# Kernel optimization log

Measured on AMD Instinct MI355X. Metric: run time of the kernel, lower is better.

## Reference

```python
import jax, jax.numpy as jnp
import numpy as np

B, S, H = 1, 2048, 1024          # batch, seq, hidden_size
INTER, K, DST, DTR = 2048, 4, 16, 64  # intermediate, kernel, ssm_state, dt_rank


def setup_inputs() -> dict:
    key = jax.random.key(0)
    ks = jax.random.split(key, 10)
    sc = 0.02
    return {
        "x": jax.random.normal(ks[0], (B, S, H), jnp.float32),
        "W_in": jax.random.normal(ks[1], (H, 2 * INTER), jnp.float32) * sc,
        "conv_w": jax.random.normal(ks[2], (K, 1, INTER), jnp.float32) * sc,
        "conv_b": jax.random.normal(ks[3], (INTER,), jnp.float32) * sc,
        "W_x": jax.random.normal(ks[4], (INTER, DTR + 2 * DST), jnp.float32) * sc,
        "W_dt": jax.random.normal(ks[5], (DTR, INTER), jnp.float32) * sc,
        "b_dt": jax.random.normal(ks[6], (INTER,), jnp.float32) * sc,
        "A_log": jax.random.normal(ks[7], (INTER, DST), jnp.float32) * sc,
        "D": jax.random.normal(ks[8], (INTER,), jnp.float32) * sc,
        "W_out": jax.random.normal(ks[9], (INTER, H), jnp.float32) * sc,
    }


def _ssm(dA, dBu, C):
    # dA, dBu: (b, s, h, d); C: (b, s, d) -> y: (b, s, h)
    xs = (jnp.moveaxis(dA, 1, 0), jnp.moveaxis(dBu, 1, 0), jnp.moveaxis(C, 1, 0))
    state0 = jnp.zeros(dA.shape[:1] + dA.shape[2:], dA.dtype)  # (b, h, d)

    def step(state, inp):
        Ai, dBui, Ci = inp  # (b,h,d), (b,h,d), (b,d)
        state = Ai * state + dBui
        y = jnp.einsum('bhd,bd->bh', state, Ci)
        return state, y

    _, ys = jax.lax.scan(step, state0, xs)  # ys: (s, b, h)
    return jnp.moveaxis(ys, 0, 1)


def reference(x, W_in, conv_w, conv_b, W_x, W_dt, b_dt, A_log, D, W_out):
    proj = x @ W_in                              # (b, s, 2*inter)
    raw, gate = jnp.split(proj, 2, axis=-1)      # each (b, s, inter)

    # causal depthwise conv over time, groups = inter
    conv = jax.lax.conv_general_dilated(
        raw, conv_w, window_strides=(1,), padding=[(K - 1, 0)],
        dimension_numbers=('NWC', 'WIO', 'NWC'), feature_group_count=INTER)
    h = jax.nn.silu(conv + conv_b)               # (b, s, inter)

    ssm_p = h @ W_x                              # (b, s, dtr + 2*d)
    ts, Bmat, C = jnp.split(ssm_p, [DTR, DTR + DST], axis=-1)
    dt = jax.nn.softplus(ts @ W_dt + b_dt)       # (b, s, inter)

    A = -jnp.exp(A_log)                          # (inter, d)
    dA = jnp.exp(dt[..., None] * A)              # (b, s, inter, d)
    dBu = dt[..., None] * Bmat[:, :, None, :] * h[..., None]  # (b, s, inter, d)

    y = _ssm(dA, dBu, C)                         # (b, s, inter)
    y = y + h * D
    y = y * jax.nn.silu(gate)
    return y @ W_out                             # (b, s, hidden)
```

## Files before the change

### kernel.cpp

```cpp
#include <hip/hip_runtime.h>
#include <math.h>

#define SEQ   2048
#define HID   1024
#define INTER 2048
#define DST   16
#define DTR   64
#define NP    96
#define NC    64
#define LCH   32
#define KS    16

typedef _Float16 f16;
typedef _Float16 f16x8 __attribute__((ext_vector_type(8)));
typedef _Float16 f16x4v __attribute__((ext_vector_type(4)));
typedef float f32x4 __attribute__((ext_vector_type(4)));

__device__ __forceinline__ float sigmoidf_(float x) { return 1.0f / (1.0f + expf(-x)); }
__device__ __forceinline__ float siluf_(float x)    { return x * sigmoidf_(x); }
__device__ __forceinline__ float softplusf_(float x){ return (x > 20.0f) ? x : log1pf(expf(x)); }

__global__ __launch_bounds__(256) void cvt_f16(const float* __restrict__ in,
                                               f16* __restrict__ out)
{
    int i = (blockIdx.x * 256 + threadIdx.x) * 4;
    float4 v = *(const float4*)&in[i];
    f16x4v o;
    o.x = (f16)v.x; o.y = (f16)v.y; o.z = (f16)v.z; o.w = (f16)v.w;
    *(f16x4v*)&out[i] = o;
}

__global__ __launch_bounds__(256) void transpose_f16(const float* __restrict__ W,
                                                     f16* __restrict__ Wt,
                                                     int K, int N)
{
    __shared__ float t[32][33];
    const int n0 = blockIdx.x * 32, k0 = blockIdx.y * 32;
    const int j = threadIdx.x & 31, i0 = threadIdx.x >> 5;
#pragma unroll
    for (int r = 0; r < 4; ++r)
        t[i0 + r * 8][j] = W[(size_t)(k0 + i0 + r * 8) * N + n0 + j];
    __syncthreads();
#pragma unroll
    for (int r = 0; r < 4; ++r)
        Wt[(size_t)(n0 + i0 + r * 8) * K + k0 + j] = (f16)t[j][i0 + r * 8];
}

template<int BM, int BN, int KK>
__global__ __launch_bounds__(256) void gemm_f16mfma(const f16* __restrict__ Ah,
                                                    const f16* __restrict__ Bt,
                                                    float* __restrict__ C,
                                                    int N)
{
    constexpr int BK = 64;
    __shared__ __align__(16) f16 As[BM * BK];
    __shared__ __align__(16) f16 Bs[BN * BK];

    const int tid = threadIdx.x;
    const int wid = tid >> 6, lane = tid & 63;
    const int wr = wid >> 1, wc = wid & 1;
    const int m0 = blockIdx.y * BM, n0 = blockIdx.x * BN;
    const int l15 = lane & 15, lhi = lane >> 4;

    constexpr int MR = BM / 32;
    constexpr int NR = BN / 32;

    f32x4 acc[MR][NR] = {};

    for (int k0 = 0; k0 < KK; k0 += BK) {
        constexpr int CA = BM * BK * 2 / 1024;
#pragma unroll
        for (int c0 = 0; c0 < CA; c0 += 4) {
            int c = c0 + wid;
            int e = c * 64 + lane;
            int row = e >> 3, seg = e & 7;
            __builtin_amdgcn_global_load_lds(
                (const __attribute__((address_space(1))) unsigned int*)
                    (Ah + (size_t)(m0 + row) * KK + k0 + seg * 8),
                (__attribute__((address_space(3))) unsigned int*)(As + c * 512),
                16, 0, 0);
        }
        constexpr int CB = BN * BK * 2 / 1024;
#pragma unroll
        for (int c0 = 0; c0 < CB; c0 += 4) {
            int c = c0 + wid;
            int e = c * 64 + lane;
            int row = e >> 3, seg = e & 7;
            __builtin_amdgcn_global_load_lds(
                (const __attribute__((address_space(1))) unsigned int*)
                    (Bt + (size_t)(n0 + row) * KK + k0 + seg * 8),
                (__attribute__((address_space(3))) unsigned int*)(Bs + c * 512),
                16, 0, 0);
        }
        __syncthreads();

#pragma unroll
        for (int kk = 0; kk < BK; kk += 32) {
            f16x8 af[MR], bf[NR];
#pragma unroll
            for (int i = 0; i < MR; ++i)
                af[i] = *(const f16x8*)&As[(wr * (BM / 2) + i * 16 + l15) * BK + kk + lhi * 8];
#pragma unroll
            for (int n = 0; n < NR; ++n)
                bf[n] = *(const f16x8*)&Bs[(wc * (BN / 2) + n * 16 + l15) * BK + kk + lhi * 8];
#pragma unroll
            for (int i = 0; i < MR; ++i)
#pragma unroll
                for (int n = 0; n < NR; ++n)
                    acc[i][n] = __builtin_amdgcn_mfma_f32_16x16x32_f16(af[i], bf[n], acc[i][n], 0, 0, 0);
        }
        __syncthreads();
    }

#pragma unroll
    for (int i = 0; i < MR; ++i)
#pragma unroll
        for (int n = 0; n < NR; ++n)
#pragma unroll
            for (int r = 0; r < 4; ++r)
                C[(size_t)(m0 + wr * (BM / 2) + i * 16 + lhi * 4 + r) * N
                  + n0 + wc * (BN / 2) + n * 16 + l15] = acc[i][n][r];
}

__global__ __launch_bounds__(256) void hwx_mfma(const f16* __restrict__ hh,
                                                const f16* __restrict__ WxT,
                                                float* __restrict__ partials)
{
    constexpr int BM = 128, BN = 96, BK = 64;
    __shared__ __align__(16) f16 As[BM * BK];
    __shared__ __align__(16) f16 Bs[BN * BK];

    const int tid = threadIdx.x;
    const int wid = tid >> 6, lane = tid & 63;
    const int wr = wid >> 1, wc = wid & 1;
    const int m0 = blockIdx.x * BM;
    const int ks = blockIdx.y;
    const int l15 = lane & 15, lhi = lane >> 4;

    constexpr int MR = 4, NR = 3;
    f32x4 acc[MR][NR] = {};

    for (int k0 = ks * 128; k0 < ks * 128 + 128; k0 += BK) {
#pragma unroll
        for (int c0 = 0; c0 < 16; c0 += 4) {
            int c = c0 + wid;
            int e = c * 64 + lane;
            int row = e >> 3, seg = e & 7;
            __builtin_amdgcn_global_load_lds(
                (const __attribute__((address_space(1))) unsigned int*)
                    (hh + (size_t)(m0 + row) * INTER + k0 + seg * 8),
                (__attribute__((address_space(3))) unsigned int*)(As + c * 512),
                16, 0, 0);
        }
#pragma unroll
        for (int c0 = 0; c0 < 12; c0 += 4) {
            int c = c0 + wid;
            int e = c * 64 + lane;
            int row = e >> 3, seg = e & 7;
            __builtin_amdgcn_global_load_lds(
                (const __attribute__((address_space(1))) unsigned int*)
                    (WxT + (size_t)row * INTER + k0 + seg * 8),
                (__attribute__((address_space(3))) unsigned int*)(Bs + c * 512),
                16, 0, 0);
        }
        __syncthreads();

#pragma unroll
        for (int kk = 0; kk < BK; kk += 32) {
            f16x8 af[MR], bf[NR];
#pragma unroll
            for (int i = 0; i < MR; ++i)
                af[i] = *(const f16x8*)&As[(wr * 64 + i * 16 + l15) * BK + kk + lhi * 8];
#pragma unroll
            for (int n = 0; n < NR; ++n)
                bf[n] = *(const f16x8*)&Bs[(wc * 48 + n * 16 + l15) * BK + kk + lhi * 8];
#pragma unroll
            for (int i = 0; i < MR; ++i)
#pragma unroll
                for (int n = 0; n < NR; ++n)
                    acc[i][n] = __builtin_amdgcn_mfma_f32_16x16x32_f16(af[i], bf[n], acc[i][n], 0, 0, 0);
        }
        __syncthreads();
    }

    float* P = partials + (size_t)ks * (SEQ * NP);
#pragma unroll
    for (int i = 0; i < MR; ++i)
#pragma unroll
        for (int n = 0; n < NR; ++n)
#pragma unroll
            for (int r = 0; r < 4; ++r)
                P[(size_t)(m0 + wr * 64 + i * 16 + lhi * 4 + r) * NP
                  + wc * 48 + n * 16 + l15] = acc[i][n][r];
}

__global__ __launch_bounds__(256) void reduce_partials(const float* __restrict__ partials,
                                                       float* __restrict__ ssm_p,
                                                       f16* __restrict__ tsh)
{
    int i = blockIdx.x * 256 + threadIdx.x;
    if (i < SEQ * NP) {
        float a = 0.0f;
#pragma unroll
        for (int c = 0; c < KS; ++c) a += partials[(size_t)c * (SEQ * NP) + i];
        ssm_p[i] = a;
        int j = i % NP;
        if (j < DTR) tsh[(size_t)(i / NP) * DTR + j] = (f16)a;
    }
}

__global__ __launch_bounds__(256) void dt_mfma(const f16* __restrict__ tsh,
                                               const f16* __restrict__ WdtT,
                                               const float* __restrict__ bdt,
                                               float* __restrict__ dtb)
{
    constexpr int BM = 128, BN = 128, BK = 64;
    __shared__ __align__(16) f16 As[BM * BK];
    __shared__ __align__(16) f16 Bs[BN * BK];

    const int tid = threadIdx.x;
    const int wid = tid >> 6, lane = tid & 63;
    const int wr = wid >> 1, wc = wid & 1;
    const int m0 = blockIdx.y * BM, n0 = blockIdx.x * BN;
    const int l15 = lane & 15, lhi = lane >> 4;

    constexpr int MR = 4, NR = 4;
    f32x4 acc[MR][NR] = {};

#pragma unroll
    for (int c0 = 0; c0 < 16; c0 += 4) {
        int c = c0 + wid;
        int e = c * 64 + lane;
        int row = e >> 3, seg = e & 7;
        __builtin_amdgcn_global_load_lds(
            (const __attribute__((address_space(1))) unsigned int*)
                (tsh + (size_t)(m0 + row) * DTR + seg * 8),
            (__attribute__((address_space(3))) unsigned int*)(As + c * 512),
            16, 0, 0);
        __builtin_amdgcn_global_load_lds(
            (const __attribute__((address_space(1))) unsigned int*)
                (WdtT + (size_t)(n0 + row) * DTR + seg * 8),
            (__attribute__((address_space(3))) unsigned int*)(Bs + c * 512),
            16, 0, 0);
    }
    __syncthreads();

#pragma unroll
    for (int kk = 0; kk < 64; kk += 32) {
        f16x8 af[MR], bf[NR];
#pragma unroll
        for (int i = 0; i < MR; ++i)
            af[i] = *(const f16x8*)&As[(wr * 64 + i * 16 + l15) * BK + kk + lhi * 8];
#pragma unroll
        for (int n = 0; n < NR; ++n)
            bf[n] = *(const f16x8*)&Bs[(wc * 64 + n * 16 + l15) * BK + kk + lhi * 8];
#pragma unroll
        for (int i = 0; i < MR; ++i)
#pragma unroll
            for (int n = 0; n < NR; ++n)
                acc[i][n] = __builtin_amdgcn_mfma_f32_16x16x32_f16(af[i], bf[n], acc[i][n], 0, 0, 0);
    }

#pragma unroll
    for (int i = 0; i < MR; ++i)
#pragma unroll
        for (int n = 0; n < NR; ++n) {
            int col = n0 + wc * 64 + n * 16 + l15;
            float bv = bdt[col];
#pragma unroll
            for (int r = 0; r < 4; ++r)
                dtb[(size_t)(m0 + wr * 64 + i * 16 + lhi * 4 + r) * INTER + col] =
                    softplusf_(acc[i][n][r] + bv);
        }
}

__global__ __launch_bounds__(256) void conv_silu(const float* __restrict__ proj,
                                                 const float* __restrict__ cw,
                                                 const float* __restrict__ cb,
                                                 float* __restrict__ hbuf,
                                                 f16* __restrict__ hh)
{
    int idx = blockIdx.x * 256 + threadIdx.x;
    int c4 = (idx & (INTER / 4 - 1)) * 4;
    int s = idx >> 9;
    float4 acc = *(const float4*)&cb[c4];
#pragma unroll
    for (int k = 0; k < 4; ++k) {
        int sp = s + k - 3;
        if (sp >= 0) {
            float4 p = *(const float4*)&proj[(size_t)sp * (2 * INTER) + c4];
            float4 w = *(const float4*)&cw[k * INTER + c4];
            acc.x = fmaf(p.x, w.x, acc.x);
            acc.y = fmaf(p.y, w.y, acc.y);
            acc.z = fmaf(p.z, w.z, acc.z);
            acc.w = fmaf(p.w, w.w, acc.w);
        }
    }
    float4 o;
    o.x = siluf_(acc.x); o.y = siluf_(acc.y); o.z = siluf_(acc.z); o.w = siluf_(acc.w);
    *(float4*)&hbuf[(size_t)idx * 4] = o;
    f16x4v h4;
    h4.x = (f16)o.x; h4.y = (f16)o.y; h4.z = (f16)o.z; h4.w = (f16)o.w;
    *(f16x4v*)&hh[(size_t)idx * 4] = h4;
}

__global__ __launch_bounds__(256) void ssm_pass1(const float* __restrict__ dtb,
                                                 const float* __restrict__ hbuf,
                                                 const float* __restrict__ ssm_p,
                                                 const float* __restrict__ A_log,
                                                 float* __restrict__ Sbuf,
                                                 float* __restrict__ Pbuf)
{
    const int h = blockIdx.x * 256 + threadIdx.x;
    const int c = blockIdx.y;
    const int s0 = c * LCH;

    __shared__ float Bs[LCH][DST];
    for (int j = threadIdx.x; j < LCH * DST; j += 256) {
        int r = j >> 4, dd = j & 15;
        Bs[r][dd] = ssm_p[(size_t)(s0 + r) * NP + DTR + dd];
    }
    __syncthreads();

    float A[DST], st[DST], P[DST];
#pragma unroll
    for (int d = 0; d < DST; ++d) {
        A[d] = -__expf(A_log[(size_t)h * DST + d]);
        st[d] = 0.0f;
        P[d] = 1.0f;
    }

    for (int r = 0; r < LCH; ++r) {
        float dtv = dtb[(size_t)(s0 + r) * INTER + h];
        float hv  = hbuf[(size_t)(s0 + r) * INTER + h];
        float dh = dtv * hv;
#pragma unroll
        for (int d = 0; d < DST; ++d) {
            float da = __expf(dtv * A[d]);
            st[d] = fmaf(da, st[d], dh * Bs[r][d]);
            P[d] *= da;
        }
    }

    size_t base = ((size_t)c * INTER + h) * DST;
#pragma unroll
    for (int d = 0; d < DST; d += 4) {
        *(float4*)&Sbuf[base + d] = make_float4(st[d], st[d+1], st[d+2], st[d+3]);
        *(float4*)&Pbuf[base + d] = make_float4(P[d], P[d+1], P[d+2], P[d+3]);
    }
}

__global__ __launch_bounds__(256) void ssm_pass2(const float* __restrict__ Sbuf,
                                                 const float* __restrict__ Pbuf,
                                                 float* __restrict__ Cin)
{
    int i = blockIdx.x * 256 + threadIdx.x;
    float carry = 0.0f;
    for (int c = 0; c < NC; ++c) {
        size_t idx = (size_t)c * (INTER * DST) + i;
        Cin[idx] = carry;
        carry = fmaf(Pbuf[idx], carry, Sbuf[idx]);
    }
}

__global__ __launch_bounds__(256) void ssm_pass3(const float* __restrict__ dtb,
                                                 const float* __restrict__ hbuf,
                                                 const float* __restrict__ ssm_p,
                                                 const float* __restrict__ proj,
                                                 const float* __restrict__ A_log,
                                                 const float* __restrict__ Dvec,
                                                 const float* __restrict__ Cin,
                                                 f16* __restrict__ yh)
{
    const int h = blockIdx.x * 256 + threadIdx.x;
    const int c = blockIdx.y;
    const int s0 = c * LCH;

    __shared__ float Bs[LCH][DST];
    __shared__ float Cs[LCH][DST];
    for (int j = threadIdx.x; j < LCH * DST; j += 256) {
        int r = j >> 4, dd = j & 15;
        Bs[r][dd] = ssm_p[(size_t)(s0 + r) * NP + DTR + dd];
        Cs[r][dd] = ssm_p[(size_t)(s0 + r) * NP + DTR + DST + dd];
    }
    __syncthreads();

    float A[DST], st[DST];
    size_t base = ((size_t)c * INTER + h) * DST;
#pragma unroll
    for (int d = 0; d < DST; ++d) {
        A[d] = -__expf(A_log[(size_t)h * DST + d]);
        st[d] = Cin[base + d];
    }
    const float Dv = Dvec[h];

    for (int r = 0; r < LCH; ++r) {
        float dtv = dtb[(size_t)(s0 + r) * INTER + h];
        float hv  = hbuf[(size_t)(s0 + r) * INTER + h];
        float g   = proj[(size_t)(s0 + r) * (2 * INTER) + INTER + h];
        float dh = dtv * hv;
        float y = 0.0f;
#pragma unroll
        for (int d = 0; d < DST; ++d) {
            float da = __expf(dtv * A[d]);
            st[d] = fmaf(da, st[d], dh * Bs[r][d]);
            y = fmaf(st[d], Cs[r][d], y);
        }
        y = fmaf(hv, Dv, y);
        yh[(size_t)(s0 + r) * INTER + h] = (f16)(y * siluf_(g));
    }
}

extern "C" void kernel_launch(void* const* d_in, const int* in_sizes, int n_in,
                              void* d_out, int out_size, void* d_ws, size_t ws_size,
                              hipStream_t stream)
{
    const float* x      = (const float*)d_in[0];
    const float* W_in   = (const float*)d_in[1];
    const float* conv_w = (const float*)d_in[2];
    const float* conv_b = (const float*)d_in[3];
    const float* W_x    = (const float*)d_in[4];
    const float* W_dt   = (const float*)d_in[5];
    const float* b_dt   = (const float*)d_in[6];
    const float* A_log  = (const float*)d_in[7];
    const float* Dv     = (const float*)d_in[8];
    const float* W_out  = (const float*)d_in[9];
    float* out = (float*)d_out;

    float* ws = (float*)d_ws;
    float* proj  = ws;
    float* hbuf  = ws + 8388608;
    float* dtb   = ws + 12582912;
    float* ssm_p = ws + 16777216;
    float* parts = ws + 16973824;
    float* Sbuf  = ws + 20119552;
    float* Pbuf  = ws + 22216704;
    float* Cin   = ws + 24313856;
    f16* yh      = (f16*)(ws + 16973824);
    f16* W_out_t = (f16*)(ws + 19070976);
    f16* xh      = (f16*)(ws + 20119552);
    f16* W_in_t  = (f16*)(ws + 21168128);
    f16* hh      = (f16*)(ws + 24313856);
    f16* WxT     = (f16*)(ws + 26411008);
    f16* tsh     = (f16*)(ws + 26509312);
    f16* WdtT    = (f16*)(ws + 26574848);

    cvt_f16<<<(SEQ * HID) / 1024, 256, 0, stream>>>(x, xh);
    transpose_f16<<<dim3(4096 / 32, HID / 32), 256, 0, stream>>>(W_in, W_in_t, HID, 2 * INTER);
    transpose_f16<<<dim3(NP / 32, INTER / 32), 256, 0, stream>>>(W_x, WxT, INTER, NP);
    transpose_f16<<<dim3(INTER / 32, DTR / 32), 256, 0, stream>>>(W_dt, WdtT, DTR, INTER);

    gemm_f16mfma<128, 128, HID><<<dim3(4096 / 128, SEQ / 128), 256, 0, stream>>>(
        xh, W_in_t, proj, 2 * INTER);

    conv_silu<<<(SEQ * INTER / 4) / 256, 256, 0, stream>>>(proj, conv_w, conv_b, hbuf, hh);

    hwx_mfma<<<dim3(SEQ / 128, KS), 256, 0, stream>>>(hh, WxT, parts);
    reduce_partials<<<(SEQ * NP + 255) / 256, 256, 0, stream>>>(parts, ssm_p, tsh);

    dt_mfma<<<dim3(INTER / 128, SEQ / 128), 256, 0, stream>>>(tsh, WdtT, b_dt, dtb);

    transpose_f16<<<dim3(HID / 32, INTER / 32), 256, 0, stream>>>(W_out, W_out_t, INTER, HID);

    ssm_pass1<<<dim3(INTER / 256, NC), 256, 0, stream>>>(dtb, hbuf, ssm_p, A_log, Sbuf, Pbuf);
    ssm_pass2<<<(INTER * DST) / 256, 256, 0, stream>>>(Sbuf, Pbuf, Cin);
    ssm_pass3<<<dim3(INTER / 256, NC), 256, 0, stream>>>(dtb, hbuf, ssm_p, proj, A_log, Dv, Cin, yh);

    gemm_f16mfma<64, 128, INTER><<<dim3(HID / 128, SEQ / 64), 256, 0, stream>>>(
        yh, W_out_t, out, HID);
}
```

Baseline: 195.9 us.

## Store intermediates in fp16 and merge weight prep into one launch

Switches the in_proj output, conv/silu activations and dt buffer from fp32 to fp16, so the fp32 hbuf copy is dropped and the SSM passes read half-width data. All conversion and transpose kernels are merged into a single prep_all launch to cut launch overhead. The conv kernel now handles 8 channels per thread. This lowers memory traffic across several stages, at the cost of extra fp16 rounding in the gate and dt values.

```diff
diff --git a/kernel.cpp b/kernel.cpp
--- a/kernel.cpp
+++ b/kernel.cpp
@@ -20,23 +20,13 @@
 __device__ __forceinline__ float siluf_(float x)    { return x * sigmoidf_(x); }
 __device__ __forceinline__ float softplusf_(float x){ return (x > 20.0f) ? x : log1pf(expf(x)); }
 
-__global__ __launch_bounds__(256) void cvt_f16(const float* __restrict__ in,
-                                               f16* __restrict__ out)
-{
-    int i = (blockIdx.x * 256 + threadIdx.x) * 4;
-    float4 v = *(const float4*)&in[i];
-    f16x4v o;
-    o.x = (f16)v.x; o.y = (f16)v.y; o.z = (f16)v.z; o.w = (f16)v.w;
-    *(f16x4v*)&out[i] = o;
-}
-
-__global__ __launch_bounds__(256) void transpose_f16(const float* __restrict__ W,
-                                                     f16* __restrict__ Wt,
-                                                     int K, int N)
+__device__ __forceinline__ void tile_transpose(const float* __restrict__ W,
+                                               f16* __restrict__ Wt,
+                                               int K, int N, int bx, int by, int tid)
 {
     __shared__ float t[32][33];
-    const int n0 = blockIdx.x * 32, k0 = blockIdx.y * 32;
-    const int j = threadIdx.x & 31, i0 = threadIdx.x >> 5;
+    const int n0 = bx * 32, k0 = by * 32;
+    const int j = tid & 31, i0 = tid >> 5;
 #pragma unroll
     for (int r = 0; r < 4; ++r)
         t[i0 + r * 8][j] = W[(size_t)(k0 + i0 + r * 8) * N + n0 + j];
@@ -46,10 +36,43 @@
         Wt[(size_t)(n0 + i0 + r * 8) * K + k0 + j] = (f16)t[j][i0 + r * 8];
 }
 
-template<int BM, int BN, int KK>
+__global__ __launch_bounds__(256) void prep_all(const float* __restrict__ x,
+                                                const float* __restrict__ W_in,
+                                                const float* __restrict__ W_out,
+                                                const float* __restrict__ W_x,
+                                                const float* __restrict__ W_dt,
+                                                f16* __restrict__ xh,
+                                                f16* __restrict__ W_in_t,
+                                                f16* __restrict__ W_out_t,
+                                                f16* __restrict__ WxT,
+                                                f16* __restrict__ WdtT)
+{
+    const int bid = blockIdx.x, tid = threadIdx.x;
+    if (bid < 2048) {
+        int i = (bid * 256 + tid) * 4;
+        float4 v = *(const float4*)&x[i];
+        f16x4v o;
+        o.x = (f16)v.x; o.y = (f16)v.y; o.z = (f16)v.z; o.w = (f16)v.w;
+        *(f16x4v*)&xh[i] = o;
+    } else if (bid < 6144) {
+        int t = bid - 2048;
+        tile_transpose(W_in, W_in_t, HID, 4096, t & 127, t >> 7, tid);
+    } else if (bid < 8192) {
+        int t = bid - 6144;
+        tile_transpose(W_out, W_out_t, INTER, HID, t & 31, t >> 5, tid);
+    } else if (bid < 8384) {
+        int t = bid - 8192;
+        tile_transpose(W_x, WxT, INTER, NP, t % 3, t / 3, tid);
+    } else {
+        int t = bid - 8384;
+        tile_transpose(W_dt, WdtT, DTR, INTER, t & 63, t >> 6, tid);
+    }
+}
+
+template<int BM, int BN, int KK, typename OutT>
 __global__ __launch_bounds__(256) void gemm_f16mfma(const f16* __restrict__ Ah,
                                                     const f16* __restrict__ Bt,
-                                                    float* __restrict__ C,
+                                                    OutT* __restrict__ C,
                                                     int N)
 {
     constexpr int BK = 64;
@@ -119,7 +142,7 @@
 #pragma unroll
             for (int r = 0; r < 4; ++r)
                 C[(size_t)(m0 + wr * (BM / 2) + i * 16 + lhi * 4 + r) * N
-                  + n0 + wc * (BN / 2) + n * 16 + l15] = acc[i][n][r];
+                  + n0 + wc * (BN / 2) + n * 16 + l15] = (OutT)acc[i][n][r];
 }
 
 __global__ __launch_bounds__(256) void hwx_mfma(const f16* __restrict__ hh,
@@ -203,16 +226,16 @@
         float a = 0.0f;
 #pragma unroll
         for (int c = 0; c < KS; ++c) a += partials[(size_t)c * (SEQ * NP) + i];
-        ssm_p[i] = a;
         int j = i % NP;
         if (j < DTR) tsh[(size_t)(i / NP) * DTR + j] = (f16)a;
+        else         ssm_p[i] = a;
     }
 }
 
 __global__ __launch_bounds__(256) void dt_mfma(const f16* __restrict__ tsh,
                                                const f16* __restrict__ WdtT,
                                                const float* __restrict__ bdt,
-                                               float* __restrict__ dtb)
+                                               f16* __restrict__ dtbh)
 {
     constexpr int BM = 128, BN = 128, BK = 64;
     __shared__ __align__(16) f16 As[BM * BK];
@@ -269,43 +292,40 @@
             float bv = bdt[col];
 #pragma unroll
             for (int r = 0; r < 4; ++r)
-                dtb[(size_t)(m0 + wr * 64 + i * 16 + lhi * 4 + r) * INTER + col] =
-                    softplusf_(acc[i][n][r] + bv);
-        }
-}
-
-__global__ __launch_bounds__(256) void conv_silu(const float* __restrict__ proj,
+                dtbh[(size_t)(m0 + wr * 64 + i * 16 + lhi * 4 + r) * INTER + col] =
+                    (f16)softplusf_(acc[i][n][r] + bv);
+        }
+}
+
+__global__ __launch_bounds__(256) void conv_silu(const f16* __restrict__ projh,
                                                  const float* __restrict__ cw,
                                                  const float* __restrict__ cb,
-                                                 float* __restrict__ hbuf,
                                                  f16* __restrict__ hh)
 {
     int idx = blockIdx.x * 256 + threadIdx.x;
-    int c4 = (idx & (INTER / 4 - 1)) * 4;
-    int s = idx >> 9;
-    float4 acc = *(const float4*)&cb[c4];
+    int c8 = (idx & (INTER / 8 - 1)) * 8;
+    int s = idx >> 8;
+    float acc[8];
+#pragma unroll
+    for (int j = 0; j < 8; ++j) acc[j] = cb[c8 + j];
 #pragma unroll
     for (int k = 0; k < 4; ++k) {
         int sp = s + k - 3;
         if (sp >= 0) {
-            float4 p = *(const float4*)&proj[(size_t)sp * (2 * INTER) + c4];
-            float4 w = *(const float4*)&cw[k * INTER + c4];
-            acc.x = fmaf(p.x, w.x, acc.x);
-            acc.y = fmaf(p.y, w.y, acc.y);
-            acc.z = fmaf(p.z, w.z, acc.z);
-            acc.w = fmaf(p.w, w.w, acc.w);
-        }
-    }
-    float4 o;
-    o.x = siluf_(acc.x); o.y = siluf_(acc.y); o.z = siluf_(acc.z); o.w = siluf_(acc.w);
-    *(float4*)&hbuf[(size_t)idx * 4] = o;
-    f16x4v h4;
-    h4.x = (f16)o.x; h4.y = (f16)o.y; h4.z = (f16)o.z; h4.w = (f16)o.w;
-    *(f16x4v*)&hh[(size_t)idx * 4] = h4;
-}
-
-__global__ __launch_bounds__(256) void ssm_pass1(const float* __restrict__ dtb,
-                                                 const float* __restrict__ hbuf,
+            f16x8 p = *(const f16x8*)&projh[(size_t)sp * (2 * INTER) + c8];
+#pragma unroll
+            for (int j = 0; j < 8; ++j)
+                acc[j] = fmaf((float)p[j], cw[k * INTER + c8 + j], acc[j]);
+        }
+    }
+    f16x8 o;
+#pragma unroll
+    for (int j = 0; j < 8; ++j) o[j] = (f16)siluf_(acc[j]);
+    *(f16x8*)&hh[(size_t)idx * 8] = o;
+}
+
+__global__ __launch_bounds__(256) void ssm_pass1(const f16* __restrict__ dtbh,
+                                                 const f16* __restrict__ hh,
                                                  const float* __restrict__ ssm_p,
                                                  const float* __restrict__ A_log,
                                                  float* __restrict__ Sbuf,
@@ -331,8 +351,8 @@
     }
 
     for (int r = 0; r < LCH; ++r) {
-        float dtv = dtb[(size_t)(s0 + r) * INTER + h];
-        float hv  = hbuf[(size_t)(s0 + r) * INTER + h];
+        float dtv = (float)dtbh[(size_t)(s0 + r) * INTER + h];
+        float hv  = (float)hh[(size_t)(s0 + r) * INTER + h];
         float dh = dtv * hv;
 #pragma unroll
         for (int d = 0; d < DST; ++d) {
@@ -363,10 +383,10 @@
     }
 }
 
-__global__ __launch_bounds__(256) void ssm_pass3(const float* __restrict__ dtb,
-                                                 const float* __restrict__ hbuf,
+__global__ __launch_bounds__(256) void ssm_pass3(const f16* __restrict__ dtbh,
+                                                 const f16* __restrict__ hh,
                                                  const float* __restrict__ ssm_p,
-                                                 const float* __restrict__ proj,
+                                                 const f16* __restrict__ projh,
                                                  const float* __restrict__ A_log,
                                                  const float* __restrict__ Dvec,
                                                  const float* __restrict__ Cin,
@@ -395,9 +415,9 @@
     const float Dv = Dvec[h];
 
     for (int r = 0; r < LCH; ++r) {
-        float dtv = dtb[(size_t)(s0 + r) * INTER + h];
-        float hv  = hbuf[(size_t)(s0 + r) * INTER + h];
-        float g   = proj[(size_t)(s0 + r) * (2 * INTER) + INTER + h];
+        float dtv = (float)dtbh[(size_t)(s0 + r) * INTER + h];
+        float hv  = (float)hh[(size_t)(s0 + r) * INTER + h];
+        float g   = (float)projh[(size_t)(s0 + r) * (2 * INTER) + INTER + h];
         float dh = dtv * hv;
         float y = 0.0f;
 #pragma unroll
@@ -428,44 +448,39 @@
     float* out = (float*)d_out;
 
     float* ws = (float*)d_ws;
-    float* proj  = ws;
-    float* hbuf  = ws + 8388608;
-    float* dtb   = ws + 12582912;
-    float* ssm_p = ws + 16777216;
-    float* parts = ws + 16973824;
-    float* Sbuf  = ws + 20119552;
-    float* Pbuf  = ws + 22216704;
-    float* Cin   = ws + 24313856;
-    f16* yh      = (f16*)(ws + 16973824);
-    f16* W_out_t = (f16*)(ws + 19070976);
-    f16* xh      = (f16*)(ws + 20119552);
-    f16* W_in_t  = (f16*)(ws + 21168128);
-    f16* hh      = (f16*)(ws + 24313856);
-    f16* WxT     = (f16*)(ws + 26411008);
-    f16* tsh     = (f16*)(ws + 26509312);
-    f16* WdtT    = (f16*)(ws + 26574848);
-
-    cvt_f16<<<(SEQ * HID) / 1024, 256, 0, stream>>>(x, xh);
-    transpose_f16<<<dim3(4096 / 32, HID / 32), 256, 0, stream>>>(W_in, W_in_t, HID, 2 * INTER);
-    transpose_f16<<<dim3(NP / 32, INTER / 32), 256, 0, stream>>>(W_x, WxT, INTER, NP);
-    transpose_f16<<<dim3(INTER / 32, DTR / 32), 256, 0, stream>>>(W_dt, WdtT, DTR, INTER);
-
-    gemm_f16mfma<128, 128, HID><<<dim3(4096 / 128, SEQ / 128), 256, 0, stream>>>(
-        xh, W_in_t, proj, 2 * INTER);
-
-    conv_silu<<<(SEQ * INTER / 4) / 256, 256, 0, stream>>>(proj, conv_w, conv_b, hbuf, hh);
+    f16*  projh  = (f16*)ws;
+    f16*  hh     = (f16*)(ws + 4194304);
+    f16*  dtbh   = (f16*)(ws + 6291456);
+    f16*  yh     = (f16*)(ws + 8388608);
+    f16*  xh     = (f16*)(ws + 10485760);
+    f16*  W_in_t = (f16*)(ws + 11534336);
+    f16*  W_out_t= (f16*)(ws + 13631488);
+    f16*  WxT    = (f16*)(ws + 14680064);
+    f16*  tsh    = (f16*)(ws + 14778368);
+    f16*  WdtT   = (f16*)(ws + 14843904);
+    float* ssm_p = ws + 14909440;
+    float* parts = ws + 15106048;
+    float* Sbuf  = ws + 18251776;
+    float* Pbuf  = ws + 20348928;
+    float* Cin   = ws + 22446080;
+
+    prep_all<<<8512, 256, 0, stream>>>(x, W_in, W_out, W_x, W_dt,
+                                       xh, W_in_t, W_out_t, WxT, WdtT);
+
+    gemm_f16mfma<128, 128, HID, f16><<<dim3(4096 / 128, SEQ / 128), 256, 0, stream>>>(
+        xh, W_in_t, projh, 2 * INTER);
+
+    conv_silu<<<(SEQ * INTER / 8) / 256, 256, 0, stream>>>(projh, conv_w, conv_b, hh);
 
     hwx_mfma<<<dim3(SEQ / 128, KS), 256, 0, stream>>>(hh, WxT, parts);
     reduce_partials<<<(SEQ * NP + 255) / 256, 256, 0, stream>>>(parts, ssm_p, tsh);
 
-    dt_mfma<<<dim3(INTER / 128, SEQ / 128), 256, 0, stream>>>(tsh, WdtT, b_dt, dtb);
-
-    transpose_f16<<<dim3(HID / 32, INTER / 32), 256, 0, stream>>>(W_out, W_out_t, INTER, HID);
-
-    ssm_pass1<<<dim3(INTER / 256, NC), 256, 0, stream>>>(dtb, hbuf, ssm_p, A_log, Sbuf, Pbuf);
+    dt_mfma<<<dim3(INTER / 128, SEQ / 128), 256, 0, stream>>>(tsh, WdtT, b_dt, dtbh);
+
+    ssm_pass1<<<dim3(INTER / 256, NC), 256, 0, stream>>>(dtbh, hh, ssm_p, A_log, Sbuf, Pbuf);
     ssm_pass2<<<(INTER * DST) / 256, 256, 0, stream>>>(Sbuf, Pbuf, Cin);
-    ssm_pass3<<<dim3(INTER / 256, NC), 256, 0, stream>>>(dtb, hbuf, ssm_p, proj, A_log, Dv, Cin, yh);
-
-    gemm_f16mfma<64, 128, INTER><<<dim3(HID / 128, SEQ / 64), 256, 0, stream>>>(
+    ssm_pass3<<<dim3(INTER / 256, NC), 256, 0, stream>>>(dtbh, hh, ssm_p, projh, A_log, Dv, Cin, yh);
+
+    gemm_f16mfma<64, 128, INTER, float><<<dim3(HID / 128, SEQ / 64), 256, 0, stream>>>(
         yh, W_out_t, out, HID);
 }
```

After: 184.0 us. 6.1% less time.
